# Performance work log

Hardware: AMD Instinct MI355X
Metric: run time of the kernel (lower is better)

Reference implementation:

```python
import jax, jax.numpy as jnp
import numpy as np

_DIR_INLIER = 0.9          # _HOUGHVOTING_DIRECTION_INLIER
_NUM_INLIER = 500          # _HOUGHVOTING_NUM_INLIER
_LABEL_THRESH = 500        # _LABEL2MASK_THRESHOL
NUM_CLASSES = 10
BS, H, W = 1, 240, 320


def setup_inputs() -> dict:
    key = jax.random.key(0)
    k_lab, k_cx, k_cy, k_nx, k_ny, k_nd = jax.random.split(key, 6)
    label = jax.random.randint(k_lab, (BS, H, W), 0, NUM_CLASSES + 1).astype(jnp.int32)
    xs = jnp.arange(W, dtype=jnp.float32)
    ys = jnp.arange(H, dtype=jnp.float32)
    xv, yv = jnp.meshgrid(xs, ys)  # [H, W] each
    # per-class ground-truth centers well inside the image so voting converges
    cxs = jax.random.uniform(k_cx, (NUM_CLASSES,), minval=40.0, maxval=W - 40.0)
    cys = jax.random.uniform(k_cy, (NUM_CLASSES,), minval=40.0, maxval=H - 40.0)
    dx = cxs[:, None, None] - xv[None]  # [C, H, W]
    dy = cys[:, None, None] - yv[None]
    nrm = jnp.sqrt(dx * dx + dy * dy) + 1e-6
    dirx = dx / nrm + 0.01 * jax.random.normal(k_nx, (NUM_CLASSES, H, W))
    diry = dy / nrm + 0.01 * jax.random.normal(k_ny, (NUM_CLASSES, H, W))
    depth = (1.0 + 0.3 * jnp.arange(NUM_CLASSES, dtype=jnp.float32))[:, None, None] \
        + 0.01 * jax.random.normal(k_nd, (NUM_CLASSES, H, W))
    cmap = jnp.stack([dirx, diry, depth], axis=1).reshape(3 * NUM_CLASSES, H, W)
    centermap = jnp.broadcast_to(cmap[None], (BS, 3 * NUM_CLASSES, H, W)).astype(jnp.float32)
    return {"label": label, "centermap": centermap}


def hough_voting(label, centermap, num_classes):
    bs, H_, W_ = label.shape
    xs = jnp.arange(W_, dtype=jnp.float32)
    ys = jnp.arange(H_, dtype=jnp.float32)
    xv, yv = jnp.meshgrid(xs, ys)            # [H, W]
    xsi = jnp.arange(W_, dtype=jnp.int32)
    all_centers, all_depths = [], []
    for b in range(bs):
        lab = label[b]
        row_c, row_d = [], []
        for cls in range(1, num_classes + 1):
            cmask = lab == cls                                    # [H, W]
            enough = cmask.sum() >= _LABEL_THRESH
            c3 = centermap[b, (cls - 1) * 3:(cls - 1) * 3 + 3]    # [3, H, W]
            slope = c3[1] / c3[0]                                  # dy/dx per pixel
            # every masked pixel votes along its line at every column x
            y_idx = jnp.round(yv[:, :, None] + slope[:, :, None] * (xs[None, None, :] - xv[:, :, None])).astype(jnp.int32)  # [H, W, W]
            valid = (y_idx >= 0) & (y_idx < H_) & cmask[:, :, None]
            bins = jnp.clip(y_idx, 0, H_ - 1) * W_ + xsi[None, None, :]
            hist = jnp.zeros(H_ * W_, jnp.float32).at[bins.ravel()].add(valid.ravel().astype(jnp.float32))
            cbin = jnp.argmax(hist)
            inlier_num = hist[cbin]
            cx = (cbin % W_).astype(jnp.float32)
            cy = (cbin // W_).astype(jnp.float32)
            # depth: mean of depth channel over direction-consistent class pixels
            disx = xv - cx
            disy = yv - cy
            dnrm = jnp.sqrt(disx * disx + disy * disy)
            dot = jnp.abs((disx / dnrm) * c3[0] + (disy / dnrm) * c3[1])  # nan at center -> compares False, as torch
            imask = (dot >= _DIR_INLIER) & cmask
            cnt = imask.sum().astype(jnp.float32)
            dsum = jnp.sum(jnp.where(imask, c3[2], 0.0))
            dmean = jnp.where(cnt > 0, dsum / jnp.maximum(cnt, 1.0), jnp.nan)
            trig = enough & (inlier_num > _NUM_INLIER)
            row_c.append(jnp.where(trig, jnp.stack([cx, cy]), jnp.zeros(2, jnp.float32)))
            row_d.append(jnp.where(trig, dmean, 0.0))
        all_centers.append(jnp.stack(row_c))
        all_depths.append(jnp.stack(row_d))
    return jnp.stack(all_centers), jnp.stack(all_depths)


def reference(label, centermap):
    return hough_voting(label, centermap, NUM_CLASSES)
```

## Files before the change

kernel.cpp:

```cpp
#include <hip/hip_runtime.h>
#include <stdint.h>

#define H 240
#define W 320
#define NPIX (H * W)
#define NCLS 10
#define COLS 4
#define BIN_BITS 20
#define BIN_MASK 0xFFFFFu
#define POIS32 0xAAAAAAAAu


__global__ __launch_bounds__(256) void k_compact(const int* __restrict__ label,
                                                 const float* __restrict__ cm,
                                                 uint32_t* __restrict__ cls_cnt,
                                                 uint2* __restrict__ list) {
    __shared__ uint32_t lcnt[NCLS];
    __shared__ uint32_t lbase[NCLS];
    int p = blockIdx.x * 256 + threadIdx.x;
    if (threadIdx.x < NCLS) lcnt[threadIdx.x] = 0;
    __syncthreads();

    int l = label[p];
    bool match = (l >= 1 && l <= NCLS);
    int cls = l - 1;
    uint32_t li = 0;
    if (match) li = atomicAdd(&lcnt[cls], 1u);
    __syncthreads();

    if (threadIdx.x < NCLS) {
        uint32_t c = lcnt[threadIdx.x];
        lbase[threadIdx.x] = c ? (atomicAdd(&cls_cnt[threadIdx.x], c) - POIS32) : 0u;
    }
    __syncthreads();

    if (match) {
        float dirx = cm[(cls * 3 + 0) * NPIX + p];
        float diry = cm[(cls * 3 + 1) * NPIX + p];
        float slope = diry / dirx;
        int y = p / W, x = p - y * W;
        uint2 e;
        e.x = (uint32_t)(x | (y << 16));
        e.y = __float_as_uint(slope);
        list[cls * NPIX + lbase[cls] + li] = e;
    }
}

__global__ __launch_bounds__(256) void k_vote(const uint32_t* __restrict__ cls_cnt,
                                              const uint2* __restrict__ list,
                                              unsigned long long* __restrict__ best) {
    int cls = blockIdx.y;
    int x0 = blockIdx.x * COLS;
    __shared__ uint32_t hist[COLS][H];
    __shared__ unsigned long long wred[4];
    for (int i = threadIdx.x; i < COLS * H; i += 256) ((uint32_t*)hist)[i] = 0;
    __syncthreads();

    int n = (int)(cls_cnt[cls] - POIS32);
    const uint2* lst = list + cls * NPIX;
    int lane = (int)(threadIdx.x & 63u);
    for (int i0 = 0; i0 < n; i0 += 256) {
        int i = i0 + (int)threadIdx.x;
        bool inb = (i < n);
        uint2 e;
        e.x = 0u; e.y = 0u;
        if (inb) e = lst[i];
        float slope = __uint_as_float(e.y);
        float xf = (float)(e.x & 0xFFFFu);
        float yf = (float)(e.x >> 16);
#pragma unroll
        for (int c = 0; c < COLS; ++c) {
            float dx = (float)(x0 + c) - xf;
            float r = rintf(yf + slope * dx);
            bool valid = inb && (r >= 0.0f) && (r <= (float)(H - 1));
            unsigned long long vm = __ballot(valid);
            if (vm == 0ull) continue;
            int bin = (int)r;
            int key = valid ? bin : -1;
            int pk = __shfl_up(key, 1);
            bool head = valid && (lane == 0 || pk != key);
            unsigned long long bmask = __ballot(head || !valid);
            if (head) {
                unsigned long long rest = (bmask >> 1) >> lane;
                int len = rest ? __ffsll(rest) : (64 - lane);
                atomicAdd(&hist[c][bin], (uint32_t)len);
            }
        }
    }
    __syncthreads();

    unsigned long long k = 0;
    for (int i = threadIdx.x; i < COLS * H; i += 256) {
        int c = i / H, y = i - c * H;
        uint32_t v = hist[c][y];
        uint32_t bin = (uint32_t)(y * W + x0 + c);
        unsigned long long key =
            ((unsigned long long)v << BIN_BITS) | (unsigned long long)(BIN_MASK - bin);
        if (key > k) k = key;
    }
#pragma unroll
    for (int off = 32; off > 0; off >>= 1) {
        unsigned long long o = __shfl_down(k, off);
        if (o > k) k = o;
    }
    if ((threadIdx.x & 63u) == 0u) wred[threadIdx.x >> 6] = k;
    __syncthreads();
    if (threadIdx.x == 0) {
        unsigned long long kk = wred[0];
#pragma unroll
        for (int w = 1; w < 4; ++w) if (wred[w] > kk) kk = wred[w];
        atomicMax((long long*)&best[cls], (long long)kk);
    }
}

__global__ __launch_bounds__(256) void k_inlier_final(
    const int* __restrict__ label, const float* __restrict__ cm,
    const uint32_t* __restrict__ cls_cnt,
    const unsigned long long* __restrict__ best,
    uint32_t* __restrict__ icnt, float* __restrict__ dsum,
    uint32_t* __restrict__ done, float* __restrict__ out) {
    __shared__ float scx[NCLS], scy[NCLS];
    __shared__ uint32_t scnt[NCLS];
    __shared__ float ssum[NCLS];
    __shared__ int slast;
    int tid = threadIdx.x;
    if (tid < NCLS) {
        unsigned long long key = best[tid];
        uint32_t bin = BIN_MASK - (uint32_t)(key & BIN_MASK);
        scx[tid] = (float)(bin % W);
        scy[tid] = (float)(bin / W);
        scnt[tid] = 0u;
        ssum[tid] = 0.0f;
    }
    __syncthreads();

    int p = blockIdx.x * 256 + tid;
    int l = label[p];
    if (l >= 1 && l <= NCLS) {
        int cls = l - 1;
        int y = p / W, x = p - y * W;
        float disx = (float)x - scx[cls];
        float disy = (float)y - scy[cls];
        float dn = sqrtf(disx * disx + disy * disy);
        if (dn > 0.0f) {
            float c0 = cm[(cls * 3 + 0) * NPIX + p];
            float c1 = cm[(cls * 3 + 1) * NPIX + p];
            float dot = fabsf((disx / dn) * c0 + (disy / dn) * c1);
            if (dot >= 0.9f) {
                atomicAdd(&scnt[cls], 1u);
                atomicAdd(&ssum[cls], cm[(cls * 3 + 2) * NPIX + p]);
            }
        }
    }
    __syncthreads();

    if (tid < NCLS) {
        if (scnt[tid]) atomicAdd(&icnt[tid], scnt[tid]);
        if (ssum[tid] != 0.0f) atomicAdd(&dsum[tid], ssum[tid]);
    }
    if (tid == 0) {
        __threadfence();
        uint32_t d = atomicAdd(done, 1u);
        slast = (d == POIS32 + (uint32_t)(gridDim.x - 1)) ? 1 : 0;
    }
    __syncthreads();

    if (slast && tid < NCLS) {
        uint32_t tc = atomicAdd(&icnt[tid], 0u) - POIS32;
        float td = atomicAdd(&dsum[tid], 0.0f);
        unsigned long long key = best[tid];
        uint32_t hv = (uint32_t)(key >> BIN_BITS);
        bool trig = ((cls_cnt[tid] - POIS32) >= 500u) && (hv > 500u);
        float c = (float)tc;
        float dm = (c > 0.0f) ? (td / fmaxf(c, 1.0f)) : __builtin_nanf("");
        out[tid * 2 + 0] = trig ? scx[tid] : 0.0f;
        out[tid * 2 + 1] = trig ? scy[tid] : 0.0f;
        out[2 * NCLS + tid] = trig ? dm : 0.0f;
    }
}

extern "C" void kernel_launch(void* const* d_in, const int* in_sizes, int n_in,
                              void* d_out, int out_size, void* d_ws, size_t ws_size,
                              hipStream_t stream) {
    const int* label = (const int*)d_in[0];
    const float* cm = (const float*)d_in[1];
    float* out = (float*)d_out;
    char* ws = (char*)d_ws;

    uint32_t* cls_cnt = (uint32_t*)(ws + 0);
    unsigned long long* best = (unsigned long long*)(ws + 64);
    uint32_t* icnt = (uint32_t*)(ws + 192);
    float* dsum = (float*)(ws + 256);
    uint32_t* done = (uint32_t*)(ws + 320);
    uint2* list = (uint2*)(ws + 512);

    k_compact<<<NPIX / 256, 256, 0, stream>>>(label, cm, cls_cnt, list);
    k_vote<<<dim3(W / COLS, NCLS), 256, 0, stream>>>(cls_cnt, list, best);
    k_inlier_final<<<NPIX / 256, 256, 0, stream>>>(label, cm, cls_cnt, best,
                                                   icnt, dsum, done, out);
}
```

Baseline: 108.0 us.

## Fuse compact, vote and inlier stages into one persistent kernel with grid barriers

Replaces three kernel launches with a single 400-block kernel that uses atomic-counter grid barriers between the compaction, voting and inlier/depth stages. Voting now covers 8 columns per block so the grid maps exactly to 400 blocks, and the per-pixel direction values are kept in registers for the inlier stage instead of being reloaded. This removes launch gaps and some global reloads. It relies on all 400 blocks being co-resident for the spin barrier, and each voting block now does twice the column work.

```diff
diff --git a/kernel.cpp b/kernel.cpp
--- a/kernel.cpp
+++ b/kernel.cpp
@@ -5,177 +5,191 @@
 #define W 320
 #define NPIX (H * W)
 #define NCLS 10
-#define COLS 4
+#define COLS 8
+#define NBLK 400
 #define BIN_BITS 20
 #define BIN_MASK 0xFFFFFu
 #define POIS32 0xAAAAAAAAu
 
 
-__global__ __launch_bounds__(256) void k_compact(const int* __restrict__ label,
-                                                 const float* __restrict__ cm,
-                                                 uint32_t* __restrict__ cls_cnt,
-                                                 uint2* __restrict__ list) {
+__device__ __forceinline__ void grid_barrier(uint32_t* bar, uint32_t target) {
+    __syncthreads();
+    if (threadIdx.x == 0) {
+        __threadfence();
+        atomicAdd(bar, 1u);
+        while ((uint32_t)(atomicAdd(bar, 0u) - POIS32) < target)
+            __builtin_amdgcn_s_sleep(16);
+        __threadfence();
+    }
+    __syncthreads();
+}
+
+__global__ __launch_bounds__(256, 2) void k_fused(
+    const int* __restrict__ label, const float* __restrict__ cm,
+    uint32_t* __restrict__ cls_cnt, uint2* __restrict__ list,
+    unsigned long long* __restrict__ best,
+    uint32_t* __restrict__ icnt, float* __restrict__ dsum,
+    uint32_t* __restrict__ done, uint32_t* __restrict__ bar,
+    float* __restrict__ out) {
     __shared__ uint32_t lcnt[NCLS];
     __shared__ uint32_t lbase[NCLS];
-    int p = blockIdx.x * 256 + threadIdx.x;
-    if (threadIdx.x < NCLS) lcnt[threadIdx.x] = 0;
-    __syncthreads();
-
-    int l = label[p];
+    __shared__ uint32_t hist[COLS][H];
+    __shared__ unsigned long long wred[4];
+    __shared__ float scx[NCLS], scy[NCLS];
+    __shared__ uint32_t scnt[NCLS];
+    __shared__ float ssum[NCLS];
+    __shared__ int slast;
+
+    const int tid = threadIdx.x;
+    const int bid = blockIdx.x;
+
+    int p = bid * 256 + tid;
+    bool live = (p < NPIX);
+    if (tid < NCLS) lcnt[tid] = 0;
+    __syncthreads();
+
+    int l = live ? label[p] : 0;
     bool match = (l >= 1 && l <= NCLS);
     int cls = l - 1;
     uint32_t li = 0;
     if (match) li = atomicAdd(&lcnt[cls], 1u);
     __syncthreads();
 
-    if (threadIdx.x < NCLS) {
-        uint32_t c = lcnt[threadIdx.x];
-        lbase[threadIdx.x] = c ? (atomicAdd(&cls_cnt[threadIdx.x], c) - POIS32) : 0u;
-    }
-    __syncthreads();
-
+    if (tid < NCLS) {
+        uint32_t c = lcnt[tid];
+        lbase[tid] = c ? (atomicAdd(&cls_cnt[tid], c) - POIS32) : 0u;
+    }
+    __syncthreads();
+
+    float dirx = 0.0f, diry = 0.0f;
+    int x = 0, y = 0;
     if (match) {
-        float dirx = cm[(cls * 3 + 0) * NPIX + p];
-        float diry = cm[(cls * 3 + 1) * NPIX + p];
+        dirx = cm[(cls * 3 + 0) * NPIX + p];
+        diry = cm[(cls * 3 + 1) * NPIX + p];
         float slope = diry / dirx;
-        int y = p / W, x = p - y * W;
+        y = p / W;
+        x = p - y * W;
         uint2 e;
         e.x = (uint32_t)(x | (y << 16));
         e.y = __float_as_uint(slope);
         list[cls * NPIX + lbase[cls] + li] = e;
     }
-}
-
-__global__ __launch_bounds__(256) void k_vote(const uint32_t* __restrict__ cls_cnt,
-                                              const uint2* __restrict__ list,
-                                              unsigned long long* __restrict__ best) {
-    int cls = blockIdx.y;
-    int x0 = blockIdx.x * COLS;
-    __shared__ uint32_t hist[COLS][H];
-    __shared__ unsigned long long wred[4];
-    for (int i = threadIdx.x; i < COLS * H; i += 256) ((uint32_t*)hist)[i] = 0;
-    __syncthreads();
-
-    int n = (int)(cls_cnt[cls] - POIS32);
-    const uint2* lst = list + cls * NPIX;
-    int lane = (int)(threadIdx.x & 63u);
-    for (int i0 = 0; i0 < n; i0 += 256) {
-        int i = i0 + (int)threadIdx.x;
-        bool inb = (i < n);
-        uint2 e;
-        e.x = 0u; e.y = 0u;
-        if (inb) e = lst[i];
-        float slope = __uint_as_float(e.y);
-        float xf = (float)(e.x & 0xFFFFu);
-        float yf = (float)(e.x >> 16);
+
+    grid_barrier(bar, NBLK);
+
+    {
+        int vcls = bid / (W / COLS);
+        int x0 = (bid % (W / COLS)) * COLS;
+        for (int i = tid; i < COLS * H; i += 256) ((uint32_t*)hist)[i] = 0;
+        __syncthreads();
+
+        int n = (int)(atomicAdd(&cls_cnt[vcls], 0u) - POIS32);
+        const uint2* lst = list + vcls * NPIX;
+        int lane = tid & 63;
+        for (int i0 = 0; i0 < n; i0 += 256) {
+            int i = i0 + tid;
+            bool inb = (i < n);
+            uint2 e;
+            e.x = 0u; e.y = 0u;
+            if (inb) e = lst[i];
+            float slope = __uint_as_float(e.y);
+            float xf = (float)(e.x & 0xFFFFu);
+            float yf = (float)(e.x >> 16);
 #pragma unroll
-        for (int c = 0; c < COLS; ++c) {
-            float dx = (float)(x0 + c) - xf;
-            float r = rintf(yf + slope * dx);
-            bool valid = inb && (r >= 0.0f) && (r <= (float)(H - 1));
-            unsigned long long vm = __ballot(valid);
-            if (vm == 0ull) continue;
-            int bin = (int)r;
-            int key = valid ? bin : -1;
-            int pk = __shfl_up(key, 1);
-            bool head = valid && (lane == 0 || pk != key);
-            unsigned long long bmask = __ballot(head || !valid);
-            if (head) {
-                unsigned long long rest = (bmask >> 1) >> lane;
-                int len = rest ? __ffsll(rest) : (64 - lane);
-                atomicAdd(&hist[c][bin], (uint32_t)len);
+            for (int c = 0; c < COLS; ++c) {
+                float dx = (float)(x0 + c) - xf;
+                float r = rintf(yf + slope * dx);
+                bool valid = inb && (r >= 0.0f) && (r <= (float)(H - 1));
+                unsigned long long vm = __ballot(valid);
+                if (vm == 0ull) continue;
+                int bin = (int)r;
+                int key = valid ? bin : -1;
+                int pk = __shfl_up(key, 1);
+                bool head = valid && (lane == 0 || pk != key);
+                unsigned long long bmask = __ballot(head || !valid);
+                if (head) {
+                    unsigned long long rest = (bmask >> 1) >> lane;
+                    int len = rest ? __ffsll(rest) : (64 - lane);
+                    atomicAdd(&hist[c][bin], (uint32_t)len);
+                }
             }
         }
-    }
-    __syncthreads();
-
-    unsigned long long k = 0;
-    for (int i = threadIdx.x; i < COLS * H; i += 256) {
-        int c = i / H, y = i - c * H;
-        uint32_t v = hist[c][y];
-        uint32_t bin = (uint32_t)(y * W + x0 + c);
-        unsigned long long key =
-            ((unsigned long long)v << BIN_BITS) | (unsigned long long)(BIN_MASK - bin);
-        if (key > k) k = key;
-    }
+        __syncthreads();
+
+        unsigned long long k = 0;
+        for (int i = tid; i < COLS * H; i += 256) {
+            int c = i / H, yy = i - c * H;
+            uint32_t v = hist[c][yy];
+            uint32_t bin = (uint32_t)(yy * W + x0 + c);
+            unsigned long long kk =
+                ((unsigned long long)v << BIN_BITS) | (unsigned long long)(BIN_MASK - bin);
+            if (kk > k) k = kk;
+        }
 #pragma unroll
-    for (int off = 32; off > 0; off >>= 1) {
-        unsigned long long o = __shfl_down(k, off);
-        if (o > k) k = o;
-    }
-    if ((threadIdx.x & 63u) == 0u) wred[threadIdx.x >> 6] = k;
-    __syncthreads();
-    if (threadIdx.x == 0) {
-        unsigned long long kk = wred[0];
+        for (int off = 32; off > 0; off >>= 1) {
+            unsigned long long o = __shfl_down(k, off);
+            if (o > k) k = o;
+        }
+        if ((tid & 63) == 0) wred[tid >> 6] = k;
+        __syncthreads();
+        if (tid == 0) {
+            unsigned long long kk = wred[0];
 #pragma unroll
-        for (int w = 1; w < 4; ++w) if (wred[w] > kk) kk = wred[w];
-        atomicMax((long long*)&best[cls], (long long)kk);
-    }
-}
-
-__global__ __launch_bounds__(256) void k_inlier_final(
-    const int* __restrict__ label, const float* __restrict__ cm,
-    const uint32_t* __restrict__ cls_cnt,
-    const unsigned long long* __restrict__ best,
-    uint32_t* __restrict__ icnt, float* __restrict__ dsum,
-    uint32_t* __restrict__ done, float* __restrict__ out) {
-    __shared__ float scx[NCLS], scy[NCLS];
-    __shared__ uint32_t scnt[NCLS];
-    __shared__ float ssum[NCLS];
-    __shared__ int slast;
-    int tid = threadIdx.x;
-    if (tid < NCLS) {
-        unsigned long long key = best[tid];
-        uint32_t bin = BIN_MASK - (uint32_t)(key & BIN_MASK);
-        scx[tid] = (float)(bin % W);
-        scy[tid] = (float)(bin / W);
-        scnt[tid] = 0u;
-        ssum[tid] = 0.0f;
-    }
-    __syncthreads();
-
-    int p = blockIdx.x * 256 + tid;
-    int l = label[p];
-    if (l >= 1 && l <= NCLS) {
-        int cls = l - 1;
-        int y = p / W, x = p - y * W;
-        float disx = (float)x - scx[cls];
-        float disy = (float)y - scy[cls];
-        float dn = sqrtf(disx * disx + disy * disy);
-        if (dn > 0.0f) {
-            float c0 = cm[(cls * 3 + 0) * NPIX + p];
-            float c1 = cm[(cls * 3 + 1) * NPIX + p];
-            float dot = fabsf((disx / dn) * c0 + (disy / dn) * c1);
-            if (dot >= 0.9f) {
-                atomicAdd(&scnt[cls], 1u);
-                atomicAdd(&ssum[cls], cm[(cls * 3 + 2) * NPIX + p]);
+            for (int w = 1; w < 4; ++w) if (wred[w] > kk) kk = wred[w];
+            atomicMax((long long*)&best[cls == cls ? vcls : vcls], (long long)kk);
+        }
+    }
+
+    grid_barrier(bar, 2u * NBLK);
+
+    {
+        if (tid < NCLS) {
+            unsigned long long key = atomicAdd(&best[tid], 0ull);
+            uint32_t bin = BIN_MASK - (uint32_t)(key & BIN_MASK);
+            scx[tid] = (float)(bin % W);
+            scy[tid] = (float)(bin / W);
+            scnt[tid] = 0u;
+            ssum[tid] = 0.0f;
+        }
+        __syncthreads();
+
+        if (match) {
+            float disx = (float)x - scx[cls];
+            float disy = (float)y - scy[cls];
+            float dn = sqrtf(disx * disx + disy * disy);
+            if (dn > 0.0f) {
+                float dot = fabsf((disx / dn) * dirx + (disy / dn) * diry);
+                if (dot >= 0.9f) {
+                    atomicAdd(&scnt[cls], 1u);
+                    atomicAdd(&ssum[cls], cm[(cls * 3 + 2) * NPIX + p]);
+                }
             }
         }
-    }
-    __syncthreads();
-
-    if (tid < NCLS) {
-        if (scnt[tid]) atomicAdd(&icnt[tid], scnt[tid]);
-        if (ssum[tid] != 0.0f) atomicAdd(&dsum[tid], ssum[tid]);
-    }
-    if (tid == 0) {
-        __threadfence();
-        uint32_t d = atomicAdd(done, 1u);
-        slast = (d == POIS32 + (uint32_t)(gridDim.x - 1)) ? 1 : 0;
-    }
-    __syncthreads();
-
-    if (slast && tid < NCLS) {
-        uint32_t tc = atomicAdd(&icnt[tid], 0u) - POIS32;
-        float td = atomicAdd(&dsum[tid], 0.0f);
-        unsigned long long key = best[tid];
-        uint32_t hv = (uint32_t)(key >> BIN_BITS);
-        bool trig = ((cls_cnt[tid] - POIS32) >= 500u) && (hv > 500u);
-        float c = (float)tc;
-        float dm = (c > 0.0f) ? (td / fmaxf(c, 1.0f)) : __builtin_nanf("");
-        out[tid * 2 + 0] = trig ? scx[tid] : 0.0f;
-        out[tid * 2 + 1] = trig ? scy[tid] : 0.0f;
-        out[2 * NCLS + tid] = trig ? dm : 0.0f;
+        __syncthreads();
+
+        if (tid < NCLS) {
+            if (scnt[tid]) atomicAdd(&icnt[tid], scnt[tid]);
+            if (ssum[tid] != 0.0f) atomicAdd(&dsum[tid], ssum[tid]);
+        }
+        if (tid == 0) {
+            __threadfence();
+            uint32_t d = atomicAdd(done, 1u);
+            slast = (d == POIS32 + (uint32_t)(NBLK - 1)) ? 1 : 0;
+        }
+        __syncthreads();
+
+        if (slast && tid < NCLS) {
+            uint32_t tc = atomicAdd(&icnt[tid], 0u) - POIS32;
+            float td = atomicAdd(&dsum[tid], 0.0f);
+            unsigned long long key = atomicAdd(&best[tid], 0ull);
+            uint32_t hv = (uint32_t)(key >> BIN_BITS);
+            bool trig = ((atomicAdd(&cls_cnt[tid], 0u) - POIS32) >= 500u) && (hv > 500u);
+            float cc = (float)tc;
+            float dm = (cc > 0.0f) ? (td / fmaxf(cc, 1.0f)) : __builtin_nanf("");
+            out[tid * 2 + 0] = trig ? scx[tid] : 0.0f;
+            out[tid * 2 + 1] = trig ? scy[tid] : 0.0f;
+            out[2 * NCLS + tid] = trig ? dm : 0.0f;
+        }
     }
 }
 
@@ -192,10 +206,9 @@
     uint32_t* icnt = (uint32_t*)(ws + 192);
     float* dsum = (float*)(ws + 256);
     uint32_t* done = (uint32_t*)(ws + 320);
+    uint32_t* bar = (uint32_t*)(ws + 384);
     uint2* list = (uint2*)(ws + 512);
 
-    k_compact<<<NPIX / 256, 256, 0, stream>>>(label, cm, cls_cnt, list);
-    k_vote<<<dim3(W / COLS, NCLS), 256, 0, stream>>>(cls_cnt, list, best);
-    k_inlier_final<<<NPIX / 256, 256, 0, stream>>>(label, cm, cls_cnt, best,
-                                                   icnt, dsum, done, out);
+    k_fused<<<NBLK, 256, 0, stream>>>(label, cm, cls_cnt, list, best,
+                                      icnt, dsum, done, bar, out);
 }
```

After: 193.0 us. 1.79x slower.
